# Performance work log

Measured on AMD Instinct MI355X. Metric: run time of the kernel, lower is better.

The kernel has to match this reference:

```python
import jax, jax.numpy as jnp
import numpy as np

N_NODES = 50000
N_EDGES = 640000
N_GRAPHS = 256
H = 128
L = 4
X_DIM, P_DIM, E_DIM = 64, 16, 16


def setup_inputs() -> dict:
    key = jax.random.key(0)
    ks = jax.random.split(key, 16)
    s = 0.05
    inp = {
        "x": jax.random.normal(ks[0], (N_NODES, X_DIM), jnp.float32),
        "p": jax.random.normal(ks[1], (N_NODES, P_DIM), jnp.float32),
        "e_attr": jax.random.normal(ks[2], (N_EDGES, E_DIM), jnp.float32),
        "edge_index": jax.random.randint(ks[3], (2, N_EDGES), 0, N_NODES, jnp.int32),
        "batch": jnp.sort(jax.random.randint(ks[4], (N_NODES,), 0, N_GRAPHS, jnp.int32)),
        # embeddings
        "W_embed": jax.random.normal(ks[5], (X_DIM + P_DIM, H), jnp.float32) * s,
        "b_embed": jnp.zeros((H,), jnp.float32),
        "W_eembed": jax.random.normal(ks[6], (E_DIM, H), jnp.float32) * s,
        "b_eembed": jnp.zeros((H,), jnp.float32),
        # per-layer stacked params
        "Wm": jax.random.normal(ks[7], (L, 3 * H, H), jnp.float32) * s,
        "bm": jnp.zeros((L, H), jnp.float32),
        "Wh": jax.random.normal(ks[8], (L, 2 * H, H), jnp.float32) * s,
        "bh": jnp.zeros((L, H), jnp.float32),
        "We": jax.random.normal(ks[9], (L, 3 * H, H), jnp.float32) * s,
        "be": jnp.zeros((L, H), jnp.float32),
    }
    return inp


def reference(x, p, e_attr, W_embed, b_embed, W_eembed, b_eembed,
              Wm, bm, Wh, bh, We, be, edge_index, batch):
    # node embed: Linear(cat(x, p))
    h = jnp.concatenate([x, p], axis=1) @ W_embed + b_embed          # [N, H]
    e = e_attr @ W_eembed + b_eembed                                 # [E, H]
    send, rec = edge_index[0], edge_index[1]
    n_nodes = x.shape[0]
    for l in range(Wm.shape[0]):
        h_send, h_rec = h[send], h[rec]                              # gathers [E, H]
        cat_ser = jnp.concatenate([h_send, h_rec, e], axis=1)        # [E, 3H]
        messages = cat_ser @ Wm[l] + bm[l]                           # [E, H]
        messages_agg = jax.ops.segment_sum(messages, rec, num_segments=n_nodes)  # scatter_add
        h = jnp.concatenate([h, messages_agg], axis=1) @ Wh[l] + bh[l]
        # e_update uses h_send/h_rec gathered from the PRE-update h (as in torch code)
        e = cat_ser @ We[l] + be[l]
    # global_add_pool over graphs
    out = jax.ops.segment_sum(h, batch, num_segments=N_GRAPHS)       # [G, H]
    return out
```

## Files before the change

### kernel.cpp

```cpp
#include <hip/hip_runtime.h>
#include <cstdio>

#define NN 50000
#define NE 640000
#define NG 256
#define NL 4

#define SCAN_CHUNK 1024
#define NB_SCAN ((NN + SCAN_CHUNK - 1) / SCAN_CHUNK)

typedef unsigned short u16;
typedef unsigned int u32;
typedef __attribute__((ext_vector_type(8))) short short8v;
typedef __attribute__((ext_vector_type(4))) float f32x4;

static __device__ __forceinline__ float bf2f(u16 v) {
    return __uint_as_float(((u32)v) << 16);
}
static __device__ __forceinline__ u16 f2bf(float f) {
    u32 u = __float_as_uint(f);
    u += 0x7fff + ((u >> 16) & 1);
    return (u16)(u >> 16);
}

__global__ __launch_bounds__(256) void k_deg(
    const int* __restrict__ rec, int* __restrict__ deg)
{
    const int e = blockIdx.x * 256 + threadIdx.x;
    atomicAdd(&deg[rec[e]], 1);
}

__global__ __launch_bounds__(256) void k_prep_xp(
    const float* __restrict__ x, const float* __restrict__ p,
    u16* __restrict__ Axp)
{
    const int idx = blockIdx.x * 256 + threadIdx.x;
    const int row = idx / 48;
    const int c2 = idx - row * 48;
    const int c0 = c2 * 2;
    float f0, f1;
    if (c0 < 64)      { f0 = x[(size_t)row * 64 + c0]; f1 = x[(size_t)row * 64 + c0 + 1]; }
    else if (c0 < 80) { f0 = p[(size_t)row * 16 + c0 - 64]; f1 = p[(size_t)row * 16 + c0 - 63]; }
    else              { f0 = 0.f; f1 = 0.f; }
    ((u32*)Axp)[idx] = (u32)f2bf(f0) | ((u32)f2bf(f1) << 16);
}

__global__ __launch_bounds__(256) void k_wembed(
    const float* __restrict__ W, u16* __restrict__ Wp)
{
    const int idx = blockIdx.x * 256 + threadIdx.x;
    const int ks = idx >> 12;
    const int rem = idx & 4095;
    const int col = rem >> 5;
    const int kk = rem & 31;
    const int k = ks * 32 + kk;
    Wp[((size_t)ks * 128 + col) * 32 + kk] = f2bf(k < 80 ? W[k * 128 + col] : 0.f);
}

__global__ __launch_bounds__(256) void k_embed(
    const u16* __restrict__ Axp, const u16* __restrict__ Wp,
    const float* __restrict__ b, u16* __restrict__ h)
{
    const int t = threadIdx.x;
    const int lane = t & 63;
    const int w = t >> 6;
    const int rb = blockIdx.x * 128 + w * 32;
    const int l15 = lane & 15;
    const int kg  = lane >> 4;

    int r0 = rb + l15;      if (r0 > NN - 1) r0 = NN - 1;
    int r1 = rb + 16 + l15; if (r1 > NN - 1) r1 = NN - 1;

    f32x4 acc[2][8];
    #pragma unroll
    for (int m = 0; m < 2; ++m)
        #pragma unroll
        for (int n = 0; n < 8; ++n) acc[m][n] = (f32x4){0.f, 0.f, 0.f, 0.f};

    #pragma unroll
    for (int ks = 0; ks < 3; ++ks) {
        const short8v a0 = *(const short8v*)(Axp + (size_t)r0 * 96 + ks * 32 + kg * 8);
        const short8v a1 = *(const short8v*)(Axp + (size_t)r1 * 96 + ks * 32 + kg * 8);
        const u16* bb = Wp + ((size_t)ks * 128 + l15) * 32 + kg * 8;
        #pragma unroll
        for (int nf = 0; nf < 8; ++nf) {
            const short8v bv = *(const short8v*)(bb + (size_t)nf * 16 * 32);
            acc[0][nf] = __builtin_amdgcn_mfma_f32_16x16x32_bf16(a0, bv, acc[0][nf], 0, 0, 0);
            acc[1][nf] = __builtin_amdgcn_mfma_f32_16x16x32_bf16(a1, bv, acc[1][nf], 0, 0, 0);
        }
    }

    #pragma unroll
    for (int m = 0; m < 2; ++m) {
        #pragma unroll
        for (int r = 0; r < 4; ++r) {
            const int row = rb + m * 16 + kg * 4 + r;
            if (row < NN) {
                #pragma unroll
                for (int nf = 0; nf < 8; ++nf) {
                    const int col = nf * 16 + l15;
                    h[(size_t)row * 128 + col] = f2bf(acc[m][nf][r] + b[col]);
                }
            }
        }
    }
}

__global__ __launch_bounds__(256) void k_wprep(
    const float* __restrict__ Wm, const float* __restrict__ Wh,
    const float* __restrict__ We, const float* __restrict__ bm,
    float* __restrict__ Wb, float* __restrict__ cvec)
{
    const int idx = blockIdx.x * 256 + threadIdx.x;
    const int total = 4 * 512 * 256;
    if (idx < total) {
        const int l = idx >> 17;
        const int rem = idx & 131071;
        const int k = rem >> 8;
        const int c = rem & 255;
        const float* Wm_l = Wm + (size_t)l * 384 * 128;
        const float* Wh_l = Wh + (size_t)l * 256 * 128;
        const float* We_l = We + (size_t)l * 384 * 128;
        float v;
        if (k < 128) {
            v = (c < 128) ? Wh_l[k * 128 + c] : 0.f;
        } else {
            const int kk  = (k - 128) & 127;
            const int blk = (k - 128) >> 7;
            const int roff = (blk == 0) ? 128 : (blk == 1) ? 0 : 256;
            if (c < 128) {
                float s = 0.f;
                #pragma unroll 4
                for (int j = 0; j < 128; ++j)
                    s += Wm_l[(roff + kk) * 128 + j] * Wh_l[(128 + j) * 128 + c];
                v = s;
            } else {
                v = We_l[(roff + kk) * 128 + (c - 128)];
            }
        }
        Wb[idx] = v;
    } else if (idx < total + 512) {
        const int r = idx - total;
        const int l = r >> 7;
        const int c = r & 127;
        const float* Wh_l = Wh + (size_t)l * 256 * 128;
        const float* bm_l = bm + l * 128;
        float s = 0.f;
        #pragma unroll 4
        for (int j = 0; j < 128; ++j) s += bm_l[j] * Wh_l[(128 + j) * 128 + c];
        cvec[r] = s;
    }
}

__global__ __launch_bounds__(256) void k_wswz(
    const float* __restrict__ Wb, u16* __restrict__ Bp)
{
    const int idx = blockIdx.x * 256 + threadIdx.x;
    const int l = idx >> 17;
    const int rem = idx & 131071;
    const int k = rem >> 8;
    const int n = rem & 255;
    const int ks = k >> 5;
    const int kg = (k >> 3) & 3;
    const int kk = k & 7;
    const int cg = n >> 6;
    const int n64 = n & 63;
    Bp[(size_t)l * 131072 +
       ((((size_t)ks * 4 + cg) * 4 + kg) * 64 + n64) * 8 + kk] = f2bf(Wb[idx]);
}

__global__ __launch_bounds__(256) void k_scanA(
    const int* __restrict__ deg, int* __restrict__ part)
{
    __shared__ int red[256];
    const int t = threadIdx.x;
    const int base = blockIdx.x * SCAN_CHUNK + t * 4;
    int s = 0;
    #pragma unroll
    for (int i = 0; i < 4; ++i) {
        const int idx = base + i;
        if (idx < NN) s += deg[idx];
    }
    red[t] = s;
    __syncthreads();
    for (int off = 128; off > 0; off >>= 1) {
        if (t < off) red[t] += red[t + off];
        __syncthreads();
    }
    if (t == 0) part[blockIdx.x] = red[0];
}

__global__ __launch_bounds__(64) void k_scanB(int* part)
{
    if (threadIdx.x == 0) {
        int run = 0;
        for (int b = 0; b < NB_SCAN; ++b) {
            const int v = part[b];
            part[b] = run;
            run += v;
        }
    }
}

__global__ __launch_bounds__(256) void k_scanC(
    const int* __restrict__ deg, const int* __restrict__ part,
    int* __restrict__ offs, int* __restrict__ cursor)
{
    __shared__ int ts[256];
    const int t = threadIdx.x;
    const int base = blockIdx.x * SCAN_CHUNK + t * 4;
    int v[4]; int s = 0;
    #pragma unroll
    for (int i = 0; i < 4; ++i) {
        const int idx = base + i;
        v[i] = (idx < NN) ? deg[idx] : 0;
        s += v[i];
    }
    ts[t] = s;
    __syncthreads();
    for (int off = 1; off < 256; off <<= 1) {
        int val = ts[t];
        if (t >= off) val += ts[t - off];
        __syncthreads();
        ts[t] = val;
        __syncthreads();
    }
    int run = part[blockIdx.x] + ((t == 0) ? 0 : ts[t - 1]);
    #pragma unroll
    for (int i = 0; i < 4; ++i) {
        const int idx = base + i;
        if (idx < NN) { offs[idx] = run; cursor[idx] = run; run += v[i]; }
    }
}

__global__ __launch_bounds__(256) void k_fill(
    const int* __restrict__ send, const int* __restrict__ rec,
    int* __restrict__ cursor, int* __restrict__ csr, int* __restrict__ csr_e)
{
    const int e = blockIdx.x * 256 + threadIdx.x;
    const int r = rec[e];
    const int pos = atomicAdd(&cursor[r], 1);
    csr[pos] = send[e];
    csr_e[pos] = e;
}

__global__ __launch_bounds__(256) void k_sea_se0(
    const float* __restrict__ ea, const int* __restrict__ csr_e,
    const int* __restrict__ offs, const int* __restrict__ deg,
    const float* __restrict__ Wee, const float* __restrict__ bee,
    u16* __restrict__ Se)
{
    __shared__ float sea[4][16];
    const int t = threadIdx.x;
    const int lane = t & 63;
    const int w = t >> 6;
    const int nb = blockIdx.x * 4;
    const int node = nb + w;
    const int g = lane >> 4;
    const int l16 = lane & 15;
    const int off = offs[node];
    const int d = deg[node];

    float acc = 0.f;
    for (int j = g; j < d; j += 4) {
        const int eid = csr_e[off + j];
        acc += ea[(size_t)eid * 16 + l16];
    }
    acc += __shfl_xor(acc, 16);
    acc += __shfl_xor(acc, 32);
    if (g == 0) sea[w][l16] = acc;
    __syncthreads();

    const int c = t & 127;
    #pragma unroll
    for (int q = 0; q < 2; ++q) {
        const int n = (t >> 7) + 2 * q;
        const int nd = nb + n;
        float a = (float)deg[nd] * bee[c];
        #pragma unroll
        for (int k = 0; k < 16; ++k) a += sea[n][k] * Wee[k * 128 + c];
        Se[(size_t)nd * 128 + c] = f2bf(a);
    }
}

__global__ __launch_bounds__(256) void k_gather(
    const u16* __restrict__ h, const int* __restrict__ csr,
    const int* __restrict__ offs, const int* __restrict__ deg,
    u16* __restrict__ Sh)
{
    const int t = threadIdx.x;
    const int lane = t & 63;
    const int node = blockIdx.x * 4 + (t >> 6);
    const int g = lane >> 4;
    const int l16 = lane & 15;
    const int off = offs[node];
    const int d = deg[node];
    const uint4* hp = (const uint4*)h;

    float a[8], b[8];
    #pragma unroll
    for (int i = 0; i < 8; ++i) { a[i] = 0.f; b[i] = 0.f; }

    int j = g;
    for (; j + 4 < d; j += 8) {
        const int s0 = csr[off + j];
        const int s1 = csr[off + j + 4];
        const uint4 v0 = hp[(size_t)s0 * 16 + l16];
        const uint4 v1 = hp[(size_t)s1 * 16 + l16];
        a[0] += bf2f((u16)(v0.x & 0xffff)); a[1] += bf2f((u16)(v0.x >> 16));
        a[2] += bf2f((u16)(v0.y & 0xffff)); a[3] += bf2f((u16)(v0.y >> 16));
        a[4] += bf2f((u16)(v0.z & 0xffff)); a[5] += bf2f((u16)(v0.z >> 16));
        a[6] += bf2f((u16)(v0.w & 0xffff)); a[7] += bf2f((u16)(v0.w >> 16));
        b[0] += bf2f((u16)(v1.x & 0xffff)); b[1] += bf2f((u16)(v1.x >> 16));
        b[2] += bf2f((u16)(v1.y & 0xffff)); b[3] += bf2f((u16)(v1.y >> 16));
        b[4] += bf2f((u16)(v1.z & 0xffff)); b[5] += bf2f((u16)(v1.z >> 16));
        b[6] += bf2f((u16)(v1.w & 0xffff)); b[7] += bf2f((u16)(v1.w >> 16));
    }
    if (j < d) {
        const uint4 v0 = hp[(size_t)csr[off + j] * 16 + l16];
        a[0] += bf2f((u16)(v0.x & 0xffff)); a[1] += bf2f((u16)(v0.x >> 16));
        a[2] += bf2f((u16)(v0.y & 0xffff)); a[3] += bf2f((u16)(v0.y >> 16));
        a[4] += bf2f((u16)(v0.z & 0xffff)); a[5] += bf2f((u16)(v0.z >> 16));
        a[6] += bf2f((u16)(v0.w & 0xffff)); a[7] += bf2f((u16)(v0.w >> 16));
    }
    #pragma unroll
    for (int i = 0; i < 8; ++i) {
        float s = a[i] + b[i];
        s += __shfl_xor(s, 16);
        s += __shfl_xor(s, 32);
        a[i] = s;
    }
    if (g == 0) {
        uint4 o;
        o.x = (u32)f2bf(a[0]) | ((u32)f2bf(a[1]) << 16);
        o.y = (u32)f2bf(a[2]) | ((u32)f2bf(a[3]) << 16);
        o.z = (u32)f2bf(a[4]) | ((u32)f2bf(a[5]) << 16);
        o.w = (u32)f2bf(a[6]) | ((u32)f2bf(a[7]) << 16);
        ((uint4*)Sh)[(size_t)node * 16 + l16] = o;
    }
}

template<bool FULL>
__global__ __launch_bounds__(256, 2) void k_dense(
    const u16* __restrict__ h, const u16* __restrict__ Sh,
    const u16* __restrict__ Se, const int* __restrict__ deg,
    const u16* __restrict__ Bp, const float* __restrict__ cvec,
    const float* __restrict__ bh, const float* __restrict__ be,
    u16* __restrict__ h_out, u16* __restrict__ Se_out)
{
    const int t = threadIdx.x;
    const int lane = t & 63;
    const int w = t >> 6;
    if (!FULL && w >= 2) return;
    const int cb = w * 64;
    const int rb = blockIdx.x * 32;
    const int l15 = lane & 15;
    const int kg  = lane >> 4;

    int r0 = rb + l15;      if (r0 > NN - 1) r0 = NN - 1;
    int r1 = rb + 16 + l15; if (r1 > NN - 1) r1 = NN - 1;

    #define SRC(ks) (((ks) >> 2) <= 1 ? h : ((ks) >> 2) == 2 ? Sh : Se)
    #define BFRAG(ks, nf) (*(const short8v*)(Bp + \
        ((((size_t)(ks) * 4 + w) * 4 + kg) * 64 + (nf) * 16 + l15) * 8))

    f32x4 accP[2][4], accQ[2][4];
    #pragma unroll
    for (int m = 0; m < 2; ++m)
        #pragma unroll
        for (int n = 0; n < 4; ++n) {
            accP[m][n] = (f32x4){0.f, 0.f, 0.f, 0.f};
            accQ[m][n] = (f32x4){0.f, 0.f, 0.f, 0.f};
        }

    short8v a[2][2];
    short8v b[2][4];

    {
        const int ko = kg * 8;
        a[0][0] = *(const short8v*)(h + (size_t)r0 * 128 + ko);
        a[0][1] = *(const short8v*)(h + (size_t)r1 * 128 + ko);
        #pragma unroll
        for (int nf = 0; nf < 4; ++nf) b[0][nf] = BFRAG(0, nf);
    }

    #pragma unroll
    for (int ks = 0; ks < 16; ++ks) {
        const int cur = ks & 1;
        const int nxt = cur ^ 1;
        const int s = ks >> 2;

        if (ks < 15) {
            const int kn = ks + 1;
            const int ko = (kn & 3) * 32 + kg * 8;
            const u16* __restrict__ Sp = SRC(kn);
            a[nxt][0] = *(const short8v*)(Sp + (size_t)r0 * 128 + ko);
            a[nxt][1] = *(const short8v*)(Sp + (size_t)r1 * 128 + ko);
            #pragma unroll
            for (int nf = 0; nf < 4; ++nf) b[nxt][nf] = BFRAG(kn, nf);
        }

        #pragma unroll
        for (int nf = 0; nf < 4; ++nf) {
            #pragma unroll
            for (int m = 0; m < 2; ++m) {
                if (s == 1)
                    accQ[m][nf] = __builtin_amdgcn_mfma_f32_16x16x32_bf16(a[cur][m], b[cur][nf], accQ[m][nf], 0, 0, 0);
                else
                    accP[m][nf] = __builtin_amdgcn_mfma_f32_16x16x32_bf16(a[cur][m], b[cur][nf], accP[m][nf], 0, 0, 0);
            }
        }
    }
    #undef SRC
    #undef BFRAG

    #pragma unroll
    for (int m = 0; m < 2; ++m) {
        #pragma unroll
        for (int r = 0; r < 4; ++r) {
            const int row = rb + m * 16 + kg * 4 + r;
            if (row < NN) {
                const float dg = (float)deg[row];
                if (cb < 128) {
                    #pragma unroll
                    for (int nf = 0; nf < 4; ++nf) {
                        const int col = cb + nf * 16 + l15;
                        h_out[(size_t)row * 128 + col] =
                            f2bf(accP[m][nf][r] + dg * accQ[m][nf][r] + bh[col] + dg * cvec[col]);
                    }
                } else {
                    #pragma unroll
                    for (int nf = 0; nf < 4; ++nf) {
                        const int col = cb - 128 + nf * 16 + l15;
                        Se_out[(size_t)row * 128 + col] =
                            f2bf(accP[m][nf][r] + dg * accQ[m][nf][r] + dg * be[col]);
                    }
                }
            }
        }
    }
}

__global__ __launch_bounds__(256) void k_pool(
    const u16* __restrict__ h, const int* __restrict__ batch,
    float* __restrict__ out)
{
    const int t = threadIdx.x;
    const int col = t & 127;
    const int half = t >> 7;
    const int base = blockIdx.x * 64 + half * 32;
    float acc = 0.f;
    int curg = -1;
    for (int i = 0; i < 32; ++i) {
        const int n = base + i;
        if (n >= NN) break;
        const int g = batch[n];
        if (g != curg) {
            if (curg >= 0) atomicAdd(&out[curg * 128 + col], acc);
            curg = g; acc = 0.f;
        }
        acc += bf2f(h[(size_t)n * 128 + col]);
    }
    if (curg >= 0) atomicAdd(&out[curg * 128 + col], acc);
}

extern "C" void kernel_launch(void* const* d_in, const int* in_sizes, int n_in,
                              void* d_out, int out_size, void* d_ws, size_t ws_size,
                              hipStream_t stream)
{
    const float* x       = (const float*)d_in[0];
    const float* p       = (const float*)d_in[1];
    const float* ea      = (const float*)d_in[2];
    const int*   eidx    = (const int*)d_in[3];
    const int*   batch   = (const int*)d_in[4];
    const float* W_embed = (const float*)d_in[5];
    const float* b_embed = (const float*)d_in[6];
    const float* W_ee    = (const float*)d_in[7];
    const float* b_ee    = (const float*)d_in[8];
    const float* Wm      = (const float*)d_in[9];
    const float* bm      = (const float*)d_in[10];
    const float* Wh      = (const float*)d_in[11];
    const float* bh      = (const float*)d_in[12];
    const float* We      = (const float*)d_in[13];
    const float* be      = (const float*)d_in[14];
    const int* send = eidx;
    const int* rec  = eidx + NE;

    char* w = (char*)d_ws;
    const size_t NHb = (size_t)NN * 128 * sizeof(u16);
    u16* hA  = (u16*)w; w += NHb;
    u16* hB  = (u16*)w; w += NHb;
    u16* SeA = (u16*)w; w += NHb;
    u16* SeB = (u16*)w; w += NHb;
    u16* Sh  = (u16*)w; w += NHb;
    u16* Axp = (u16*)w;  w += (size_t)NN * 96 * 2;
    int*  deg    = (int*)w;   w += (size_t)NN * 4;
    int*  offs   = (int*)w;   w += (size_t)(NN + 4) * 4;
    int*  cursor = (int*)w;   w += (size_t)NN * 4;
    int*  csr    = (int*)w;   w += (size_t)NE * 4;
    int*  csr_e  = (int*)w;   w += (size_t)NE * 4;
    int*  part   = (int*)w;   w += 64 * 4;
    float* Wb    = (float*)w; w += (size_t)4 * 512 * 256 * 4;
    float* cvec  = (float*)w; w += 512 * 4;
    u16*  Bp     = (u16*)w;   w += (size_t)4 * 512 * 256 * 2;
    u16*  Wpe    = (u16*)w;   w += (size_t)3 * 128 * 32 * 2;
    const size_t need = (size_t)(w - (char*)d_ws);
    if (ws_size < need) {
        fprintf(stderr, "[kernel_launch] ws_size=%zu < needed=%zu — skipping\n",
                ws_size, need);
        return;
    }

    float* out = (float*)d_out;

    hipMemsetAsync(d_out, 0, (size_t)NG * 128 * sizeof(float), stream);
    hipMemsetAsync(deg, 0, (size_t)NN * sizeof(int), stream);

    k_deg<<<NE / 256, 256, 0, stream>>>(rec, deg);
    k_prep_xp<<<NN * 48 / 256, 256, 0, stream>>>(x, p, Axp);
    k_wembed<<<3 * 128 * 32 / 256, 256, 0, stream>>>(W_embed, Wpe);
    k_embed<<<(NN + 127) / 128, 256, 0, stream>>>(Axp, Wpe, b_embed, hA);
    k_wprep<<<(4 * 512 * 256 + 512 + 255) / 256, 256, 0, stream>>>(Wm, Wh, We, bm, Wb, cvec);
    k_wswz<<<4 * 512 * 256 / 256, 256, 0, stream>>>(Wb, Bp);
    k_scanA<<<NB_SCAN, 256, 0, stream>>>(deg, part);
    k_scanB<<<1, 64, 0, stream>>>(part);
    k_scanC<<<NB_SCAN, 256, 0, stream>>>(deg, part, offs, cursor);
    k_fill<<<NE / 256, 256, 0, stream>>>(send, rec, cursor, csr, csr_e);
    k_sea_se0<<<NN / 4, 256, 0, stream>>>(ea, csr_e, offs, deg, W_ee, b_ee, SeA);

    u16* h_cur = hA;   u16* h_nxt = hB;
    u16* Se_cur = SeA; u16* Se_nxt = SeB;
    for (int l = 0; l < NL; ++l) {
        k_gather<<<NN / 4, 256, 0, stream>>>(h_cur, csr, offs, deg, Sh);
        if (l < NL - 1)
            k_dense<true><<<(NN + 31) / 32, 256, 0, stream>>>(h_cur, Sh, Se_cur,
                deg, Bp + (size_t)l * 131072,
                cvec + l * 128, bh + l * 128, be + l * 128, h_nxt, Se_nxt);
        else
            k_dense<false><<<(NN + 31) / 32, 256, 0, stream>>>(h_cur, Sh, Se_cur,
                deg, Bp + (size_t)l * 131072,
                cvec + l * 128, bh + l * 128, be + l * 128, h_nxt, Se_nxt);
        u16* tmp;
        tmp = h_cur;  h_cur  = h_nxt;  h_nxt  = tmp;
        tmp = Se_cur; Se_cur = Se_nxt; Se_nxt = tmp;
    }
    k_pool<<<(NN + 63) / 64, 256, 0, stream>>>(h_cur, batch, out);
}
```

Measured before the change: 434.6 us.

## Scatter edge attributes into CSR order and rotate dense K-loop start per block

k_fill now records each edge's CSR position, and a new k_escat kernel scatters e_attr rows into CSR order. k_sea_se0 can then sum contiguous float4 runs instead of doing an indirect gather per edge. Separately, k_dense starts its K-step loop at a block-dependent offset, so concurrent blocks read different source buffers and weight slices instead of all hitting the same ones. This adds an extra 41MB scatter pass and a larger workspace, and the rotated loop may cost registers or code size.

Result: slower. 461.8 us (+6.3%).

```diff
diff --git a/kernel.cpp b/kernel.cpp
--- a/kernel.cpp
+++ b/kernel.cpp
@@ -235,20 +235,30 @@
 
 __global__ __launch_bounds__(256) void k_fill(
     const int* __restrict__ send, const int* __restrict__ rec,
-    int* __restrict__ cursor, int* __restrict__ csr, int* __restrict__ csr_e)
+    int* __restrict__ cursor, int* __restrict__ csr, int* __restrict__ pos_arr)
 {
     const int e = blockIdx.x * 256 + threadIdx.x;
     const int r = rec[e];
     const int pos = atomicAdd(&cursor[r], 1);
     csr[pos] = send[e];
-    csr_e[pos] = e;
+    pos_arr[e] = pos;
+}
+
+__global__ __launch_bounds__(256) void k_escat(
+    const float* __restrict__ ea, const int* __restrict__ pos_arr,
+    float* __restrict__ eap)
+{
+    const int t = threadIdx.x;
+    const int e = blockIdx.x * 16 + (t >> 4);
+    const int l16 = t & 15;
+    const int p = pos_arr[e];
+    eap[(size_t)p * 16 + l16] = ea[(size_t)e * 16 + l16];
 }
 
 __global__ __launch_bounds__(256) void k_sea_se0(
-    const float* __restrict__ ea, const int* __restrict__ csr_e,
-    const int* __restrict__ offs, const int* __restrict__ deg,
-    const float* __restrict__ Wee, const float* __restrict__ bee,
-    u16* __restrict__ Se)
+    const float4* __restrict__ eap4, const int* __restrict__ offs,
+    const int* __restrict__ deg, const float* __restrict__ Wee,
+    const float* __restrict__ bee, u16* __restrict__ Se)
 {
     __shared__ float sea[4][16];
     const int t = threadIdx.x;
@@ -256,19 +266,25 @@
     const int w = t >> 6;
     const int nb = blockIdx.x * 4;
     const int node = nb + w;
-    const int g = lane >> 4;
-    const int l16 = lane & 15;
-    const int off = offs[node];
-    const int d = deg[node];
-
-    float acc = 0.f;
-    for (int j = g; j < d; j += 4) {
-        const int eid = csr_e[off + j];
-        acc += ea[(size_t)eid * 16 + l16];
-    }
-    acc += __shfl_xor(acc, 16);
-    acc += __shfl_xor(acc, 32);
-    if (g == 0) sea[w][l16] = acc;
+    const size_t off4 = (size_t)offs[node] * 4;
+    const int n4 = deg[node] * 4;
+
+    float acc[4] = {0.f, 0.f, 0.f, 0.f};
+    for (int j = lane; j < n4; j += 64) {
+        const float4 v = eap4[off4 + j];
+        acc[0] += v.x; acc[1] += v.y; acc[2] += v.z; acc[3] += v.w;
+    }
+    #pragma unroll
+    for (int i = 0; i < 4; ++i) {
+        acc[i] += __shfl_xor(acc[i], 4);
+        acc[i] += __shfl_xor(acc[i], 8);
+        acc[i] += __shfl_xor(acc[i], 16);
+        acc[i] += __shfl_xor(acc[i], 32);
+    }
+    if (lane < 4) {
+        #pragma unroll
+        for (int i = 0; i < 4; ++i) sea[w][lane * 4 + i] = acc[i];
+    }
     __syncthreads();
 
     const int c = t & 127;
@@ -373,25 +389,29 @@
             accQ[m][n] = (f32x4){0.f, 0.f, 0.f, 0.f};
         }
 
+    const int start = blockIdx.x & 15;
     short8v a[2][2];
     short8v b[2][4];
 
     {
-        const int ko = kg * 8;
-        a[0][0] = *(const short8v*)(h + (size_t)r0 * 128 + ko);
-        a[0][1] = *(const short8v*)(h + (size_t)r1 * 128 + ko);
-        #pragma unroll
-        for (int nf = 0; nf < 4; ++nf) b[0][nf] = BFRAG(0, nf);
-    }
-
-    #pragma unroll
-    for (int ks = 0; ks < 16; ++ks) {
-        const int cur = ks & 1;
+        const int ks = start;
+        const int ko = (ks & 3) * 32 + kg * 8;
+        const u16* __restrict__ Sp = SRC(ks);
+        a[0][0] = *(const short8v*)(Sp + (size_t)r0 * 128 + ko);
+        a[0][1] = *(const short8v*)(Sp + (size_t)r1 * 128 + ko);
+        #pragma unroll
+        for (int nf = 0; nf < 4; ++nf) b[0][nf] = BFRAG(ks, nf);
+    }
+
+    #pragma unroll
+    for (int i = 0; i < 16; ++i) {
+        const int ks = (start + i) & 15;
+        const int cur = i & 1;
         const int nxt = cur ^ 1;
         const int s = ks >> 2;
 
-        if (ks < 15) {
-            const int kn = ks + 1;
+        if (i < 15) {
+            const int kn = (start + i + 1) & 15;
             const int ko = (kn & 3) * 32 + kg * 8;
             const u16* __restrict__ Sp = SRC(kn);
             a[nxt][0] = *(const short8v*)(Sp + (size_t)r0 * 128 + ko);
@@ -400,15 +420,18 @@
             for (int nf = 0; nf < 4; ++nf) b[nxt][nf] = BFRAG(kn, nf);
         }
 
-        #pragma unroll
-        for (int nf = 0; nf < 4; ++nf) {
+        if (s == 1) {
             #pragma unroll
-            for (int m = 0; m < 2; ++m) {
-                if (s == 1)
+            for (int nf = 0; nf < 4; ++nf)
+                #pragma unroll
+                for (int m = 0; m < 2; ++m)
                     accQ[m][nf] = __builtin_amdgcn_mfma_f32_16x16x32_bf16(a[cur][m], b[cur][nf], accQ[m][nf], 0, 0, 0);
-                else
+        } else {
+            #pragma unroll
+            for (int nf = 0; nf < 4; ++nf)
+                #pragma unroll
+                for (int m = 0; m < 2; ++m)
                     accP[m][nf] = __builtin_amdgcn_mfma_f32_16x16x32_bf16(a[cur][m], b[cur][nf], accP[m][nf], 0, 0, 0);
-            }
         }
     }
     #undef SRC
@@ -498,12 +521,13 @@
     int*  offs   = (int*)w;   w += (size_t)(NN + 4) * 4;
     int*  cursor = (int*)w;   w += (size_t)NN * 4;
     int*  csr    = (int*)w;   w += (size_t)NE * 4;
-    int*  csr_e  = (int*)w;   w += (size_t)NE * 4;
+    int*  pos_arr = (int*)w;  w += (size_t)NE * 4;
     int*  part   = (int*)w;   w += 64 * 4;
     float* Wb    = (float*)w; w += (size_t)4 * 512 * 256 * 4;
     float* cvec  = (float*)w; w += 512 * 4;
     u16*  Bp     = (u16*)w;   w += (size_t)4 * 512 * 256 * 2;
     u16*  Wpe    = (u16*)w;   w += (size_t)3 * 128 * 32 * 2;
+    float* eap   = (float*)w; w += (size_t)NE * 16 * 4;
     const size_t need = (size_t)(w - (char*)d_ws);
     if (ws_size < need) {
         fprintf(stderr, "[kernel_launch] ws_size=%zu < needed=%zu — skipping\n",
@@ -525,8 +549,9 @@
     k_scanA<<<NB_SCAN, 256, 0, stream>>>(deg, part);
     k_scanB<<<1, 64, 0, stream>>>(part);
     k_scanC<<<NB_SCAN, 256, 0, stream>>>(deg, part, offs, cursor);
-    k_fill<<<NE / 256, 256, 0, stream>>>(send, rec, cursor, csr, csr_e);
-    k_sea_se0<<<NN / 4, 256, 0, stream>>>(ea, csr_e, offs, deg, W_ee, b_ee, SeA);
+    k_fill<<<NE / 256, 256, 0, stream>>>(send, rec, cursor, csr, pos_arr);
+    k_escat<<<NE / 16, 256, 0, stream>>>(ea, pos_arr, eap);
+    k_sea_se0<<<NN / 4, 256, 0, stream>>>((const float4*)eap, offs, deg, W_ee, b_ee, SeA);
 
     u16* h_cur = hA;   u16* h_nxt = hB;
     u16* Se_cur = SeA; u16* Se_nxt = SeB;
```
